# Optimization experiments

Hardware: AMD Instinct MI355X
Metric: run time of the kernel (lower is better)

The kernel has to match this reference:

```python
import jax, jax.numpy as jnp
import numpy as np

HIDDEN = 1024
NUM_HEADS = 16
HEAD_DIM = HIDDEN // NUM_HEADS
WINDOW = 512


def setup_inputs() -> dict:
    key = jax.random.key(0)
    ks = jax.random.split(key, 6)
    b, s = 2, 4096
    x = jax.random.normal(ks[0], (b, s, HIDDEN), dtype=jnp.float32)
    attention_mask = jnp.ones((b, s), dtype=jnp.int32)
    scale = 1.0 / np.sqrt(HIDDEN)
    Wq = jax.random.normal(ks[1], (HIDDEN, HIDDEN), dtype=jnp.float32) * scale
    Wk = jax.random.normal(ks[2], (HIDDEN, HIDDEN), dtype=jnp.float32) * scale
    Wv = jax.random.normal(ks[3], (HIDDEN, HIDDEN), dtype=jnp.float32) * scale
    Wo = jax.random.normal(ks[4], (HIDDEN, HIDDEN), dtype=jnp.float32) * scale
    return {"x": x, "attention_mask": attention_mask,
            "Wq": Wq, "Wk": Wk, "Wv": Wv, "Wo": Wo}


def reference(x, attention_mask, Wq, Wk, Wv, Wo):
    b, s, d = x.shape
    # nn.Linear computes x @ W.T
    q = (x @ Wq.T).reshape(b, s, NUM_HEADS, HEAD_DIM).transpose(0, 2, 1, 3)
    k = (x @ Wk.T).reshape(b, s, NUM_HEADS, HEAD_DIM).transpose(0, 2, 1, 3)
    v = (x @ Wv.T).reshape(b, s, NUM_HEADS, HEAD_DIM).transpose(0, 2, 1, 3)
    # [b,h,s,s] scores
    scores = jnp.einsum('bhqd,bhkd->bhqk', q, k) / np.sqrt(HEAD_DIM)
    # causal sliding-window mask: allow j <= i and j >= i - window + 1
    i = jnp.arange(s)[:, None]
    j = jnp.arange(s)[None, :]
    window_mask = (j <= i) & (j >= i - WINDOW + 1)  # [s,s]
    neg_inf = jnp.finfo(scores.dtype).min
    scores = jnp.where(window_mask[None, None], scores, neg_inf)
    pad = attention_mask.astype(bool)[:, None, None, :]  # [b,1,1,s]
    scores = jnp.where(pad, scores, neg_inf)
    probs = jax.nn.softmax(scores, axis=-1)
    out = jnp.einsum('bhqk,bhkd->bhqd', probs, v)
    out = out.transpose(0, 2, 1, 3).reshape(b, s, d)
    return out @ Wo.T
```

## Files before the change

### kernel.cpp

```cpp
#include <hip/hip_runtime.h>
#include <cstdint>
#include <cstddef>

#define HID 1024
#define SEQ 4096
#define NB  2
#define NH  16
#define HD  64
#define WIN 512
#define TOK (NB*SEQ)

typedef _Float16 f16x8 __attribute__((ext_vector_type(8)));
typedef _Float16 f16x4 __attribute__((ext_vector_type(4)));
typedef float    f32x4 __attribute__((ext_vector_type(4)));

__global__ __launch_bounds__(256)
void convertX_kernel(const float* __restrict__ src, _Float16* __restrict__ dst) {
  const int i = (blockIdx.x * 256 + threadIdx.x) * 8;
  f32x4 a = *(const f32x4*)(src + i);
  f32x4 b = *(const f32x4*)(src + i + 4);
  f16x8 o;
#pragma unroll
  for (int r = 0; r < 4; ++r) { o[r] = (_Float16)a[r]; o[r+4] = (_Float16)b[r]; }
  *(f16x8*)(dst + i) = o;
}

__global__ __launch_bounds__(256)
void convertW_kernel(const float* __restrict__ w0, const float* __restrict__ w1,
                     const float* __restrict__ w2, const float* __restrict__ w3,
                     _Float16* __restrict__ dst) {
  const int z = blockIdx.z;
  const float* s = (z == 0) ? w0 : (z == 1) ? w1 : (z == 2) ? w2 : w3;
  _Float16* d = dst + (size_t)z * HID * HID;
  const int i = (blockIdx.x * 256 + threadIdx.x) * 8;
  f32x4 a = *(const f32x4*)(s + i);
  f32x4 b = *(const f32x4*)(s + i + 4);
  f16x8 o;
#pragma unroll
  for (int r = 0; r < 4; ++r) { o[r] = (_Float16)a[r]; o[r+4] = (_Float16)b[r]; }
  *(f16x8*)(d + i) = o;
}

__device__ __forceinline__ void gload16(const void* g, void* lds) {
  __builtin_amdgcn_global_load_lds(
      (__attribute__((address_space(1))) void*)(void*)g,
      (__attribute__((address_space(3))) void*)lds, 16, 0, 0);
}

__device__ __forceinline__ void gemm_mainloop(
    const _Float16* __restrict__ A, const _Float16* __restrict__ W,
    _Float16* sA, _Float16* sB, f32x4 (&acc)[4][4], int m0, int n0) {
  const int tid  = threadIdx.x;
  const int lane = tid & 63;
  const int wave = tid >> 6;
  const int wm = wave >> 1, wn = wave & 1;
  const int l15 = lane & 15, quad = lane >> 4;

  const int o0 = tid * 16;
  const int o1 = o0 + 4096;
  const _Float16* a0 = A + (size_t)(m0 + (o0 >> 6)) * HID + ((o0 & 63) >> 1);
  const _Float16* a1 = A + (size_t)(m0 + (o1 >> 6)) * HID + ((o1 & 63) >> 1);
  const _Float16* w0 = W + (size_t)(n0 + (o0 >> 6)) * HID + ((o0 & 63) >> 1);
  const _Float16* w1 = W + (size_t)(n0 + (o1 >> 6)) * HID + ((o1 & 63) >> 1);
  _Float16* la0 = sA + (o0 >> 1);
  _Float16* la1 = sA + (o1 >> 1);
  _Float16* lb0 = sB + (o0 >> 1);
  _Float16* lb1 = sB + (o1 >> 1);

  const int aoff = (wm*64 + l15)*32 + quad*8;
  const int boff = (wn*64 + l15)*32 + quad*8;

  for (int k0 = 0; k0 < HID; k0 += 32) {
    __syncthreads();
    gload16(a0 + k0, la0);
    gload16(a1 + k0, la1);
    gload16(w0 + k0, lb0);
    gload16(w1 + k0, lb1);
    __syncthreads();
    f16x8 af[4], wf[4];
#pragma unroll
    for (int t = 0; t < 4; ++t) {
      af[t] = *(const f16x8*)(sA + aoff + t*512);
      wf[t] = *(const f16x8*)(sB + boff + t*512);
    }
#pragma unroll
    for (int i = 0; i < 4; ++i)
#pragma unroll
      for (int j = 0; j < 4; ++j)
        acc[i][j] = __builtin_amdgcn_mfma_f32_16x16x32_f16(af[i], wf[j], acc[i][j], 0, 0, 0);
  }
}

__global__ __launch_bounds__(256, 2)
void gemm_qkv_kernel(const _Float16* __restrict__ X,
                     const _Float16* __restrict__ Wh,
                     _Float16* __restrict__ Q,
                     _Float16* __restrict__ Kb,
                     _Float16* __restrict__ Vt) {
  __shared__ __align__(16) _Float16 sA[128*32];
  __shared__ __align__(16) _Float16 sB[128*32];
  const int z = blockIdx.z;
  const _Float16* W = Wh + (size_t)z * HID * HID;
  const int m0 = blockIdx.y * 128;
  const int n0 = blockIdx.x * 128;
  f32x4 acc[4][4] = {};
  gemm_mainloop(X, W, sA, sB, acc, m0, n0);

  const int tid  = threadIdx.x;
  const int lane = tid & 63;
  const int wave = tid >> 6;
  const int wm = wave >> 1, wn = wave & 1;
  const int l15 = lane & 15, quad = lane >> 4;

  if (z < 2) {
    _Float16* C = (z == 0) ? Q : Kb;
    const float scl = (z == 0) ? 0.125f : 1.0f;
#pragma unroll
    for (int tm = 0; tm < 4; ++tm)
#pragma unroll
      for (int tn = 0; tn < 4; ++tn) {
        const int row = m0 + wm*64 + tm*16 + quad*4;
        const int col = n0 + wn*64 + tn*16 + l15;
#pragma unroll
        for (int r = 0; r < 4; ++r)
          C[(size_t)(row + r)*HID + col] = (_Float16)(acc[tm][tn][r] * scl);
      }
  } else {
#pragma unroll
    for (int tm = 0; tm < 4; ++tm)
#pragma unroll
      for (int tn = 0; tn < 4; ++tn) {
        const int row = m0 + wm*64 + tm*16 + quad*4;
        const int col = n0 + wn*64 + tn*16 + l15;
        f16x4 v;
#pragma unroll
        for (int r = 0; r < 4; ++r) v[r] = (_Float16)acc[tm][tn][r];
        *(f16x4*)(Vt + (size_t)col*TOK + row) = v;
      }
  }
}

__global__ __launch_bounds__(256, 2)
void gemm_o_kernel(const _Float16* __restrict__ A,
                   const _Float16* __restrict__ Wo,
                   float* __restrict__ C) {
  __shared__ __align__(16) _Float16 sA[128*32];
  __shared__ __align__(16) _Float16 sB[128*32];
  const int m0 = blockIdx.y * 128;
  const int n0 = blockIdx.x * 128;
  f32x4 acc[4][4] = {};
  gemm_mainloop(A, Wo, sA, sB, acc, m0, n0);

  const int tid  = threadIdx.x;
  const int lane = tid & 63;
  const int wave = tid >> 6;
  const int wm = wave >> 1, wn = wave & 1;
  const int l15 = lane & 15, quad = lane >> 4;
#pragma unroll
  for (int tm = 0; tm < 4; ++tm)
#pragma unroll
    for (int tn = 0; tn < 4; ++tn) {
      const int row = m0 + wm*64 + tm*16 + quad*4;
      const int col = n0 + wn*64 + tn*16 + l15;
#pragma unroll
      for (int r = 0; r < 4; ++r)
        C[(size_t)(row + r)*HID + col] = acc[tm][tn][r];
    }
}

__global__ __launch_bounds__(256, 2)
void attn_kernel(const _Float16* __restrict__ Q, const _Float16* __restrict__ Kb,
                 const _Float16* __restrict__ Vt, const int* __restrict__ AM,
                 _Float16* __restrict__ O) {
  __shared__ __align__(16) _Float16 sK[64*64];
  __shared__ __align__(16) _Float16 sV[64*64];
  __shared__ __align__(16) _Float16 sP[4*32*64];
  __shared__ int sOK;

  const int qt = blockIdx.x, h = blockIdx.y, b = blockIdx.z;
  const int tid  = threadIdx.x;
  const int lane = tid & 63, wave = tid >> 6;
  const int l15 = lane & 15, quad = lane >> 4;

  const int q0 = qt * 128;
  const int qw = q0 + wave * 32;

  const int swz = l15 & 7;
  const int cA8 = ((quad ^ swz) << 3);
  const int cB8 = (((quad + 4) ^ swz) << 3);

  f16x8 qf[2][2];
#pragma unroll
  for (int ns = 0; ns < 2; ++ns) {
    const size_t qb = (size_t)(b*SEQ + qw + ns*16 + l15)*HID + h*HD + quad*8;
    qf[ns][0] = *(const f16x8*)(Q + qb);
    qf[ns][1] = *(const f16x8*)(Q + qb + 32);
  }

  const int kt_hi = 2*qt + 1;
  int kt_lo = 2*qt - 8; if (kt_lo < 0) kt_lo = 0;

  if (tid == 0) sOK = 1;
  __syncthreads();
  {
    int ok = 1;
    const int jbeg = kt_lo*64, jend = (kt_hi + 1)*64;
    for (int j = jbeg + tid; j < jend; j += 256) ok &= (AM[b*SEQ + j] != 0);
    if (!ok) sOK = 0;
  }
  __syncthreads();
  const bool allok = (sOK != 0);

  const int prow = tid >> 3;
  const int pc   = tid & 7;
  const int pco  = ((pc ^ (prow & 7)) << 3);
  f16x8 pk0, pk1, pv0, pv1;
  {
    const int j0 = kt_lo * 64;
    const _Float16* kp = Kb + (size_t)(b*SEQ + j0 + prow)*HID + h*HD + pco;
    pk0 = *(const f16x8*)kp;
    pk1 = *(const f16x8*)(kp + (size_t)32*HID);
    const _Float16* vp = Vt + (size_t)(h*HD + prow)*TOK + b*SEQ + j0 + pco;
    pv0 = *(const f16x8*)vp;
    pv1 = *(const f16x8*)(vp + (size_t)32*TOK);
  }

  float m_run[2] = {-1e20f, -1e20f}, l_run[2] = {0.0f, 0.0f};
  f32x4 o[4][2] = {};
  _Float16* myP = sP + wave * (32*64);

  for (int kt = kt_lo; kt <= kt_hi; ++kt) {
    const int j0 = kt * 64;
    __syncthreads();
    *(f16x8*)(sK + tid*8)        = pk0;
    *(f16x8*)(sK + tid*8 + 2048) = pk1;
    *(f16x8*)(sV + tid*8)        = pv0;
    *(f16x8*)(sV + tid*8 + 2048) = pv1;
    __syncthreads();
    if (kt < kt_hi) {
      int jn = (kt + 1) * 64; if (jn > SEQ - 64) jn = SEQ - 64;
      const _Float16* kp = Kb + (size_t)(b*SEQ + jn + prow)*HID + h*HD + pco;
      pk0 = *(const f16x8*)kp;
      pk1 = *(const f16x8*)(kp + (size_t)32*HID);
      const _Float16* vp = Vt + (size_t)(h*HD + prow)*TOK + b*SEQ + jn + pco;
      pv0 = *(const f16x8*)vp;
      pv1 = *(const f16x8*)(vp + (size_t)32*TOK);
    }

    f32x4 sc[4][2] = {};
#pragma unroll
    for (int t = 0; t < 4; ++t) {
      const f16x8 kf0 = *(const f16x8*)(sK + (t*16 + l15)*64 + cA8);
      const f16x8 kf1 = *(const f16x8*)(sK + (t*16 + l15)*64 + cB8);
      sc[t][0] = __builtin_amdgcn_mfma_f32_16x16x32_f16(kf0, qf[0][0], sc[t][0], 0, 0, 0);
      sc[t][0] = __builtin_amdgcn_mfma_f32_16x16x32_f16(kf1, qf[0][1], sc[t][0], 0, 0, 0);
      sc[t][1] = __builtin_amdgcn_mfma_f32_16x16x32_f16(kf0, qf[1][0], sc[t][1], 0, 0, 0);
      sc[t][1] = __builtin_amdgcn_mfma_f32_16x16x32_f16(kf1, qf[1][1], sc[t][1], 0, 0, 0);
    }

    if (!allok) {
#pragma unroll
      for (int t = 0; t < 4; ++t)
#pragma unroll
        for (int r = 0; r < 4; ++r) {
          const float ad = (AM[b*SEQ + j0 + t*16 + quad*4 + r] == 0) ? -2e30f : 0.0f;
          sc[t][0][r] += ad;
          sc[t][1][r] += ad;
        }
    }

#pragma unroll
    for (int ns = 0; ns < 2; ++ns) {
      const int i = qw + ns*16 + l15;
      float mx = -1e30f;
#pragma unroll
      for (int t = 0; t < 4; ++t)
#pragma unroll
        for (int r = 0; r < 4; ++r) {
          const int j = j0 + t*16 + quad*4 + r;
          const bool valid = (unsigned)(i - j) < WIN;
          const float s = valid ? sc[t][ns][r] : -1e30f;
          sc[t][ns][r] = s;
          mx = fmaxf(mx, s);
        }
      mx = fmaxf(mx, __shfl_xor(mx, 16, 64));
      mx = fmaxf(mx, __shfl_xor(mx, 32, 64));
      const float mnew = fmaxf(m_run[ns], mx);
      const float alpha = __expf(m_run[ns] - mnew);
      m_run[ns] = mnew;
      float sum = 0.0f;
#pragma unroll
      for (int t = 0; t < 4; ++t) {
        f16x4 pv;
#pragma unroll
        for (int r = 0; r < 4; ++r) {
          const float p = __expf(sc[t][ns][r] - mnew);
          sum += p;
          pv[r] = (_Float16)p;
        }
        const int paddr = (ns*16 + l15)*64 + (((2*t + (quad >> 1)) ^ swz) << 3) + (quad & 1)*4;
        *(f16x4*)(myP + paddr) = pv;
      }
      sum += __shfl_xor(sum, 16, 64);
      sum += __shfl_xor(sum, 32, 64);
      l_run[ns] = l_run[ns]*alpha + sum;
#pragma unroll
      for (int dt = 0; dt < 4; ++dt)
#pragma unroll
        for (int r = 0; r < 4; ++r) o[dt][ns][r] *= alpha;
    }

    const f16x8 pf00 = *(const f16x8*)(myP + l15*64 + cA8);
    const f16x8 pf01 = *(const f16x8*)(myP + l15*64 + cB8);
    const f16x8 pf10 = *(const f16x8*)(myP + (16 + l15)*64 + cA8);
    const f16x8 pf11 = *(const f16x8*)(myP + (16 + l15)*64 + cB8);
#pragma unroll
    for (int dt = 0; dt < 4; ++dt) {
      const f16x8 vf0 = *(const f16x8*)(sV + (dt*16 + l15)*64 + cA8);
      const f16x8 vf1 = *(const f16x8*)(sV + (dt*16 + l15)*64 + cB8);
      o[dt][0] = __builtin_amdgcn_mfma_f32_16x16x32_f16(vf0, pf00, o[dt][0], 0, 0, 0);
      o[dt][0] = __builtin_amdgcn_mfma_f32_16x16x32_f16(vf1, pf01, o[dt][0], 0, 0, 0);
      o[dt][1] = __builtin_amdgcn_mfma_f32_16x16x32_f16(vf0, pf10, o[dt][1], 0, 0, 0);
      o[dt][1] = __builtin_amdgcn_mfma_f32_16x16x32_f16(vf1, pf11, o[dt][1], 0, 0, 0);
    }
  }

  const float inv[2] = {1.0f / fmaxf(l_run[0], 1e-30f), 1.0f / fmaxf(l_run[1], 1e-30f)};
#pragma unroll
  for (int ns = 0; ns < 2; ++ns) {
    const size_t ob = (size_t)(b*SEQ + qw + ns*16 + l15)*HID + h*HD + quad*4;
#pragma unroll
    for (int dt = 0; dt < 4; ++dt) {
      f16x4 v;
#pragma unroll
      for (int r = 0; r < 4; ++r) v[r] = (_Float16)(o[dt][ns][r] * inv[ns]);
      *(f16x4*)(O + ob + dt*16) = v;
    }
  }
}

extern "C" void kernel_launch(void* const* d_in, const int* in_sizes, int n_in,
                              void* d_out, int out_size, void* d_ws, size_t ws_size,
                              hipStream_t stream) {
  const float* X  = (const float*)d_in[0];
  const int*   AM = (const int*)d_in[1];
  const float* Wq = (const float*)d_in[2];
  const float* Wk = (const float*)d_in[3];
  const float* Wv = (const float*)d_in[4];
  const float* Wo = (const float*)d_in[5];
  float* out = (float*)d_out;

  _Float16* Xh = (_Float16*)d_ws;
  _Float16* Wh = Xh + (size_t)TOK*HID;
  _Float16* Qb = Wh + (size_t)4*HID*HID;
  _Float16* Kb = Qb + (size_t)TOK*HID;
  _Float16* Vt = Kb + (size_t)TOK*HID;
  _Float16* AO = Vt + (size_t)TOK*HID;

  dim3 blk(256);
  convertX_kernel<<<dim3((TOK*HID)/(256*8)), blk, 0, stream>>>(X, Xh);
  convertW_kernel<<<dim3((HID*HID)/(256*8), 1, 4), blk, 0, stream>>>(Wq, Wk, Wv, Wo, Wh);
  gemm_qkv_kernel<<<dim3(HID/128, TOK/128, 3), blk, 0, stream>>>(Xh, Wh, Qb, Kb, Vt);
  attn_kernel<<<dim3(SEQ/128, NH, NB), blk, 0, stream>>>(Qb, Kb, Vt, AM, AO);
  gemm_o_kernel<<<dim3(HID/128, TOK/128, 1), blk, 0, stream>>>(AO, Wh + (size_t)3*HID*HID, out);
}
```

Before: 248.3 us.

## Double GEMM K-step to 64 and remap block indices for XCD-aware locality

The GEMM mainloop now loads a K-slice of 64 per iteration into doubled shared buffers, which halves the number of barrier pairs per tile. All three main kernels switch to a 1D grid with a custom mapping that groups blocks sharing the same weight columns or the same head/batch onto the same blockIdx modulo 8. The intent is that blocks landing on the same XCD reuse data in its L2 cache. In exchange, shared memory per block doubles (16KB to 32KB), which may affect occupancy, and the index arithmetic is more complex.

```diff
diff --git a/kernel.cpp b/kernel.cpp
--- a/kernel.cpp
+++ b/kernel.cpp
@@ -70,24 +70,32 @@
   const int aoff = (wm*64 + l15)*32 + quad*8;
   const int boff = (wn*64 + l15)*32 + quad*8;
 
-  for (int k0 = 0; k0 < HID; k0 += 32) {
+  for (int k0 = 0; k0 < HID; k0 += 64) {
     __syncthreads();
-    gload16(a0 + k0, la0);
-    gload16(a1 + k0, la1);
-    gload16(w0 + k0, lb0);
-    gload16(w1 + k0, lb1);
+    gload16(a0 + k0,      la0);
+    gload16(a1 + k0,      la1);
+    gload16(a0 + k0 + 32, la0 + 4096);
+    gload16(a1 + k0 + 32, la1 + 4096);
+    gload16(w0 + k0,      lb0);
+    gload16(w1 + k0,      lb1);
+    gload16(w0 + k0 + 32, lb0 + 4096);
+    gload16(w1 + k0 + 32, lb1 + 4096);
     __syncthreads();
-    f16x8 af[4], wf[4];
-#pragma unroll
-    for (int t = 0; t < 4; ++t) {
-      af[t] = *(const f16x8*)(sA + aoff + t*512);
-      wf[t] = *(const f16x8*)(sB + boff + t*512);
-    }
-#pragma unroll
-    for (int i = 0; i < 4; ++i)
-#pragma unroll
-      for (int j = 0; j < 4; ++j)
-        acc[i][j] = __builtin_amdgcn_mfma_f32_16x16x32_f16(af[i], wf[j], acc[i][j], 0, 0, 0);
+#pragma unroll
+    for (int s = 0; s < 2; ++s) {
+      const int sb = s * 4096;
+      f16x8 af[4], wf[4];
+#pragma unroll
+      for (int t = 0; t < 4; ++t) {
+        af[t] = *(const f16x8*)(sA + sb + aoff + t*512);
+        wf[t] = *(const f16x8*)(sB + sb + boff + t*512);
+      }
+#pragma unroll
+      for (int i = 0; i < 4; ++i)
+#pragma unroll
+        for (int j = 0; j < 4; ++j)
+          acc[i][j] = __builtin_amdgcn_mfma_f32_16x16x32_f16(af[i], wf[j], acc[i][j], 0, 0, 0);
+    }
   }
 }
 
@@ -97,12 +105,16 @@
                      _Float16* __restrict__ Q,
                      _Float16* __restrict__ Kb,
                      _Float16* __restrict__ Vt) {
-  __shared__ __align__(16) _Float16 sA[128*32];
-  __shared__ __align__(16) _Float16 sB[128*32];
-  const int z = blockIdx.z;
+  __shared__ __align__(16) _Float16 sA[128*64];
+  __shared__ __align__(16) _Float16 sB[128*64];
+  const int i = blockIdx.x;
+  const int g = i & 7;
+  const int j = i >> 3;
+  const int c = g*3 + (j >> 6);
+  const int z = c % 3;
+  const int n0 = (c / 3) * 128;
+  const int m0 = (j & 63) * 128;
   const _Float16* W = Wh + (size_t)z * HID * HID;
-  const int m0 = blockIdx.y * 128;
-  const int n0 = blockIdx.x * 128;
   f32x4 acc[4][4] = {};
   gemm_mainloop(X, W, sA, sB, acc, m0, n0);
 
@@ -144,10 +156,11 @@
 void gemm_o_kernel(const _Float16* __restrict__ A,
                    const _Float16* __restrict__ Wo,
                    float* __restrict__ C) {
-  __shared__ __align__(16) _Float16 sA[128*32];
-  __shared__ __align__(16) _Float16 sB[128*32];
-  const int m0 = blockIdx.y * 128;
-  const int n0 = blockIdx.x * 128;
+  __shared__ __align__(16) _Float16 sA[128*64];
+  __shared__ __align__(16) _Float16 sB[128*64];
+  const int i = blockIdx.x;
+  const int n0 = (i & 7) * 128;
+  const int m0 = (i >> 3) * 128;
   f32x4 acc[4][4] = {};
   gemm_mainloop(A, Wo, sA, sB, acc, m0, n0);
 
@@ -177,7 +190,13 @@
   __shared__ __align__(16) _Float16 sP[4*32*64];
   __shared__ int sOK;
 
-  const int qt = blockIdx.x, h = blockIdx.y, b = blockIdx.z;
+  const int bi = blockIdx.x;
+  const int g  = bi & 7;
+  const int jj = bi >> 3;
+  const int combo = g*4 + (jj >> 5);
+  const int h = combo & 15, b = combo >> 4;
+  const int qt = jj & 31;
+
   const int tid  = threadIdx.x;
   const int lane = tid & 63, wave = tid >> 6;
   const int l15 = lane & 15, quad = lane >> 4;
@@ -360,7 +379,7 @@
   dim3 blk(256);
   convertX_kernel<<<dim3((TOK*HID)/(256*8)), blk, 0, stream>>>(X, Xh);
   convertW_kernel<<<dim3((HID*HID)/(256*8), 1, 4), blk, 0, stream>>>(Wq, Wk, Wv, Wo, Wh);
-  gemm_qkv_kernel<<<dim3(HID/128, TOK/128, 3), blk, 0, stream>>>(Xh, Wh, Qb, Kb, Vt);
-  attn_kernel<<<dim3(SEQ/128, NH, NB), blk, 0, stream>>>(Qb, Kb, Vt, AM, AO);
-  gemm_o_kernel<<<dim3(HID/128, TOK/128, 1), blk, 0, stream>>>(AO, Wh + (size_t)3*HID*HID, out);
-}
+  gemm_qkv_kernel<<<dim3(1536), blk, 0, stream>>>(Xh, Wh, Qb, Kb, Vt);
+  attn_kernel<<<dim3(1024), blk, 0, stream>>>(Qb, Kb, Vt, AM, AO);
+  gemm_o_kernel<<<dim3(512), blk, 0, stream>>>(AO, Wh + (size_t)3*HID*HID, out);
+}
```

Measured after the change: 241.6 us. 1.03x faster.
